# Optimization experiments

Measured on AMD Instinct MI355X. Metric: run time of the kernel, lower is better.

## Reference

```python
import jax, jax.numpy as jnp
import numpy as np

B, T = 64, 512
V, E = 512, 128      # dsl vocab, embedding dim
IMG = 1024           # img_repr_size
H = 512              # dsl_hidden_dim
A = 512              # n_actions
PAD = 0


def setup_inputs() -> dict:
    key = jax.random.key(0)
    ks = jax.random.split(key, 10)
    x1 = jax.random.normal(ks[0], (B, IMG), dtype=jnp.float32)
    x2 = jax.random.randint(ks[1], (B, T), 0, V)
    x2_lens = jax.random.randint(ks[2], (B,), 1, T + 1)
    s_in = 1.0 / np.sqrt(E + IMG)
    s_h = 1.0 / np.sqrt(H)
    emb = jax.random.normal(ks[3], (V, E), dtype=jnp.float32)
    emb = emb.at[PAD].set(0.0)  # padding_idx row is zero
    W_ih = jax.random.uniform(ks[4], (4 * H, E + IMG), jnp.float32, -s_h, s_h)
    W_hh = jax.random.uniform(ks[5], (4 * H, H), jnp.float32, -s_h, s_h)
    b_ih = jax.random.uniform(ks[6], (4 * H,), jnp.float32, -s_h, s_h)
    b_hh = jax.random.uniform(ks[7], (4 * H,), jnp.float32, -s_h, s_h)
    W_act = jax.random.uniform(ks[8], (A, H), jnp.float32, -s_h, s_h)
    b_act = jax.random.uniform(ks[9], (A,), jnp.float32, -s_h, s_h)
    return {"x1": x1, "x2": x2, "x2_lens": x2_lens, "emb": emb,
            "W_ih": W_ih, "W_hh": W_hh, "b_ih": b_ih, "b_hh": b_hh,
            "W_act": W_act, "b_act": b_act}


def reference(x1, x2, x2_lens, emb, W_ih, W_hh, b_ih, b_hh, W_act, b_act):
    # embed tokens and concat image repr at every timestep: [B, T, IMG+E]
    tok = emb[x2]                                        # [B, T, E]
    img = jnp.broadcast_to(x1[:, None, :], (B, T, IMG))  # [B, T, IMG]
    x = jnp.concatenate([img, tok], axis=2)              # [B, T, IMG+E]

    # precompute input-to-gate projections in one big GEMM
    gx = jnp.einsum('bti,gi->tbg', x, W_ih) + b_ih       # [T, B, 4H]

    def step(carry, gx_t):
        h, c = carry
        g = gx_t + h @ W_hh.T + b_hh                     # [B, 4H]
        i, f, gg, o = jnp.split(g, 4, axis=1)            # torch gate order i,f,g,o
        i = jax.nn.sigmoid(i); f = jax.nn.sigmoid(f)
        gg = jnp.tanh(gg); o = jax.nn.sigmoid(o)
        c = f * c + i * gg
        h = o * jnp.tanh(c)
        return (h, c), h

    h0 = jnp.zeros((B, H), jnp.float32)
    c0 = jnp.zeros((B, H), jnp.float32)
    (_, _), hs = jax.lax.scan(step, (h0, c0), gx)        # hs: [T, B, H]

    # hn = hidden state at each sequence's true last step (packed-seq semantics)
    idx = (x2_lens - 1).astype(jnp.int32)                # [B]
    hn = jnp.take_along_axis(hs.transpose(1, 0, 2), idx[:, None, None], axis=1)[:, 0, :]  # [B, H]

    nt = hn @ W_act.T + b_act                            # [B, A]
    return nt
```

## Files before the change

kernel.cpp:

```cpp
#include <hip/hip_runtime.h>
#include <cstdint>
#include <cstddef>


typedef _Float16     f16x8 __attribute__((ext_vector_type(8)));
typedef _Float16     f16x2 __attribute__((ext_vector_type(2)));
typedef float        f32x4 __attribute__((ext_vector_type(4)));
typedef float        f32x2 __attribute__((ext_vector_type(2)));
typedef unsigned int u32x4 __attribute__((ext_vector_type(4)));

#define TPB 256
#define NWG 64

#define WS_GX0   0
#define WS_P     524288
#define WS_HN    4718592
#define WS_HBUF  4849664
#define WS_FLAGS 4980736

__device__ __forceinline__ float sigm_(float x) { return 1.f / (1.f + __expf(-x)); }
__device__ __forceinline__ float tanh_(float x) {
    const float e = __expf(-2.f * fabsf(x));
    return copysignf((1.f - e) / (1.f + e), x);
}

__device__ __forceinline__ void st_ic_u32(unsigned int* p, unsigned int v) {
    __hip_atomic_store(p, v, __ATOMIC_RELAXED, __HIP_MEMORY_SCOPE_AGENT);
}
__device__ __forceinline__ unsigned int ld_ic_u32(const unsigned int* p) {
    return __hip_atomic_load(p, __ATOMIC_RELAXED, __HIP_MEMORY_SCOPE_AGENT);
}

__global__ void gemm_nt_bias(const float* __restrict__ A, int lda,
                             const float* __restrict__ B, int ldb,
                             float* __restrict__ C, int ldc, int K,
                             const float* __restrict__ bias1,
                             const float* __restrict__ bias2)
{
    __shared__ float As[32 * 68];
    __shared__ float Bs[32 * 68];
    const int tid = threadIdx.x;
    const int m0 = blockIdx.y * 64, n0 = blockIdx.x * 64;
    const int kchunk = K / gridDim.z;
    const int kbeg = blockIdx.z * kchunk, kend = kbeg + kchunk;
    const int tr = tid >> 4, tc = tid & 15;
    float acc[4][4] = {};

    for (int k0 = kbeg; k0 < kend; k0 += 32) {
        __syncthreads();
        #pragma unroll
        for (int idx = tid; idx < 2048; idx += TPB) {
            const int r = idx >> 5, kk = idx & 31;
            As[kk * 68 + r] = A[(size_t)(m0 + r) * lda + k0 + kk];
            Bs[kk * 68 + r] = B[(size_t)(n0 + r) * ldb + k0 + kk];
        }
        __syncthreads();
        #pragma unroll
        for (int kk = 0; kk < 32; ++kk) {
            const f32x4 a = *(const f32x4*)&As[kk * 68 + tr * 4];
            const f32x4 b = *(const f32x4*)&Bs[kk * 68 + tc * 4];
            #pragma unroll
            for (int i = 0; i < 4; ++i)
                #pragma unroll
                for (int j = 0; j < 4; ++j)
                    acc[i][j] = fmaf(a[i], b[j], acc[i][j]);
        }
    }

    const bool split = (gridDim.z > 1);
    #pragma unroll
    for (int i = 0; i < 4; ++i) {
        const int m = m0 + tr * 4 + i;
        #pragma unroll
        for (int j = 0; j < 4; ++j) {
            const int n = n0 + tc * 4 + j;
            float v = acc[i][j];
            if (blockIdx.z == 0) {
                if (bias1) v += bias1[n];
                if (bias2) v += bias2[n];
            }
            if (split) atomicAdd(&C[(size_t)m * ldc + n], v);
            else       C[(size_t)m * ldc + n] = v;
        }
    }
}

__global__ void __launch_bounds__(TPB, 1)
lstm_seq(const float* __restrict__ Whh,
         const float* __restrict__ GX0,
         const float* __restrict__ P,
         const int*   __restrict__ x2,
         const int*   __restrict__ lens,
         _Float16*    hbuf,
         float*       __restrict__ hn,
         unsigned int* flags)
{
    __shared__ float Spart[4 * 128 * 20];

    const int tid = threadIdx.x, wg = blockIdx.x;
    const int lane = tid & 63, wv = tid >> 6;
    const int BG = wg >> 4;
    const int CG = wg & 15;
    const int m16 = lane & 15, q = lane >> 4;

    const int bl  = tid >> 4;
    const int cq  = (tid & 15) * 2;
    const int b   = BG * 16 + bl;
    const int col = CG * 32 + cq;
    const int last = lens[b] - 1;
    const int* toks = x2 + b * 512;

    f32x2 gxv[4];
    {
        const float* gx = GX0 + (size_t)b * 2048 + col;
        #pragma unroll
        for (int g = 0; g < 4; ++g) gxv[g] = *(const f32x2*)(gx + g * 512);
    }

    { f16x2 z; z[0] = (_Float16)0.f; z[1] = (_Float16)0.f;
      st_ic_u32((unsigned int*)(hbuf + b * 512 + col),
                __builtin_bit_cast(unsigned int, z)); }
    __syncthreads();
    unsigned int* myflag = flags + (size_t)wg * 64;
    if (tid == 0) st_ic_u32(myflag, 1u);

    const unsigned int* pollp =
        flags + (size_t)(BG * 16 + wv * 4 + (lane & 3)) * 64;

    f16x8 bfr[8][4];
    #pragma unroll
    for (int n = 0; n < 8; ++n) {
        const int rr = n * 16 + m16;
        const int gr = (rr >> 5) * 512 + CG * 32 + (rr & 31);
        const float* wrow = Whh + (size_t)gr * 512 + wv * 128 + q * 8;
        #pragma unroll
        for (int ks = 0; ks < 4; ++ks) {
            const f32x4 w0 = *(const f32x4*)(wrow + ks * 32);
            const f32x4 w1 = *(const f32x4*)(wrow + ks * 32 + 4);
            f16x8 bv;
            #pragma unroll
            for (int e = 0; e < 4; ++e) {
                bv[e]     = (_Float16)w0[e];
                bv[4 + e] = (_Float16)w1[e];
            }
            bfr[n][ks] = bv;
        }
    }

    int tok1;
    f32x2 ppv[4];
    {
        const int tok0 = toks[0];
        const float* pp = P + (size_t)tok0 * 2048 + col;
        #pragma unroll
        for (int g = 0; g < 4; ++g) ppv[g] = *(const f32x2*)(pp + g * 512);
        tok1 = toks[1];
    }

    float c0 = 0.f, c1 = 0.f;

    for (int t = 0; t < 512; ++t) {
        const unsigned int tgt = (unsigned int)(t + 1);

        while (true) {
            const unsigned int v = ld_ic_u32(pollp);
            if (__all((int)(v >= tgt))) break;
        }
        asm volatile("" ::: "memory");

        const _Float16* hsrc = hbuf + (size_t)(t & 1) * (64 * 512);
        _Float16*       hdst = hbuf + (size_t)((t + 1) & 1) * (64 * 512);

        u32x4 a0, a1, a2, a3;
        {
            const _Float16* ap =
                hsrc + (BG * 16 + m16) * 512 + wv * 128 + q * 8;
            asm volatile(
                "global_load_dwordx4 %0, %4, off sc1\n\t"
                "global_load_dwordx4 %1, %4, off offset:64 sc1\n\t"
                "global_load_dwordx4 %2, %4, off offset:128 sc1\n\t"
                "global_load_dwordx4 %3, %4, off offset:192 sc1\n\t"
                "s_waitcnt vmcnt(0)"
                : "=&v"(a0), "=&v"(a1), "=&v"(a2), "=&v"(a3)
                : "v"(ap)
                : "memory");
        }
        f16x8 af[4] = {
            __builtin_bit_cast(f16x8, a0), __builtin_bit_cast(f16x8, a1),
            __builtin_bit_cast(f16x8, a2), __builtin_bit_cast(f16x8, a3)
        };

        f32x4 acc[8] = {};
        #pragma unroll
        for (int ks = 0; ks < 4; ++ks)
            #pragma unroll
            for (int n = 0; n < 8; ++n)
                acc[n] = __builtin_amdgcn_mfma_f32_16x16x32_f16(
                    af[ks], bfr[n][ks], acc[n], 0, 0, 0);

        {
            const int cl = lane & 15, r0 = (lane >> 4) * 4;
            #pragma unroll
            for (int n = 0; n < 8; ++n)
                *(f32x4*)&Spart[(wv * 128 + n * 16 + cl) * 20 + r0] = acc[n];
        }
        __syncthreads();

        f32x2 sv[4];
        #pragma unroll
        for (int g = 0; g < 4; ++g) {
            f32x2 s = {0.f, 0.f};
            #pragma unroll
            for (int w = 0; w < 4; ++w) {
                const int base = (w * 128 + g * 32 + cq) * 20 + bl;
                s[0] += Spart[base];
                s[1] += Spart[base + 20];
            }
            sv[g] = s;
        }

        float hv[2];
        #pragma unroll
        for (int p = 0; p < 2; ++p) {
            const float iv = sigm_(sv[0][p] + gxv[0][p] + ppv[0][p]);
            const float fv = sigm_(sv[1][p] + gxv[1][p] + ppv[1][p]);
            const float gv = tanh_(sv[2][p] + gxv[2][p] + ppv[2][p]);
            const float ov = sigm_(sv[3][p] + gxv[3][p] + ppv[3][p]);
            float& c = p ? c1 : c0;
            c = fv * c + iv * gv;
            hv[p] = ov * tanh_(c);
        }

        f16x2 hh; hh[0] = (_Float16)hv[0]; hh[1] = (_Float16)hv[1];
        st_ic_u32((unsigned int*)(hdst + b * 512 + col),
                  __builtin_bit_cast(unsigned int, hh));
        if (t == last) {
            f32x2 o; o[0] = hv[0]; o[1] = hv[1];
            *(f32x2*)(hn + (size_t)b * 512 + col) = o;
        }

        __syncthreads();
        if (tid == 0) st_ic_u32(myflag, (unsigned int)(t + 2));

        {
            const float* pn = P + (size_t)tok1 * 2048 + col;
            #pragma unroll
            for (int g = 0; g < 4; ++g)
                ppv[g] = *(const f32x2*)(pn + g * 512);
            tok1 = toks[t < 510 ? t + 2 : 511];
        }
    }
}

extern "C" void kernel_launch(void* const* d_in, const int* in_sizes, int n_in,
                              void* d_out, int out_size, void* d_ws, size_t ws_size,
                              hipStream_t stream)
{
    const float* x1    = (const float*)d_in[0];
    const int*   x2    = (const int*)  d_in[1];
    const int*   lens  = (const int*)  d_in[2];
    const float* emb   = (const float*)d_in[3];
    const float* W_ih  = (const float*)d_in[4];
    const float* W_hh  = (const float*)d_in[5];
    const float* b_ih  = (const float*)d_in[6];
    const float* b_hh  = (const float*)d_in[7];
    const float* W_act = (const float*)d_in[8];
    const float* b_act = (const float*)d_in[9];
    float* out = (float*)d_out;

    char* ws = (char*)d_ws;
    float*        GX0   = (float*)(ws + WS_GX0);
    float*        P     = (float*)(ws + WS_P);
    float*        hn    = (float*)(ws + WS_HN);
    _Float16*     hbuf  = (_Float16*)(ws + WS_HBUF);
    unsigned int* flags = (unsigned int*)(ws + WS_FLAGS);

    hipMemsetAsync(flags, 0, 16384, stream);
    hipMemsetAsync(GX0, 0, 64 * 2048 * sizeof(float), stream);
    hipMemsetAsync(out, 0, 64 * 512 * sizeof(float), stream);

    gemm_nt_bias<<<dim3(32, 1, 4), TPB, 0, stream>>>(
        x1, 1024, W_ih, 1152, GX0, 2048, 1024, b_ih, b_hh);
    gemm_nt_bias<<<dim3(32, 8, 1), TPB, 0, stream>>>(
        emb, 128, W_ih + 1024, 1152, P, 2048, 128, nullptr, nullptr);

    lstm_seq<<<NWG, TPB, 0, stream>>>(W_hh, GX0, P, x2, lens, hbuf, hn, flags);

    gemm_nt_bias<<<dim3(8, 1, 4), TPB, 0, stream>>>(
        hn, 512, W_act, 512, out, 512, 512, b_act, nullptr);
}
```

Baseline: 1.454 ms.

## Pack step tag with hidden values to replace flag polling and barrier

```diff
diff --git a/kernel.cpp b/kernel.cpp
--- a/kernel.cpp
+++ b/kernel.cpp
@@ -16,19 +16,11 @@
 #define WS_P     524288
 #define WS_HN    4718592
 #define WS_HBUF  4849664
-#define WS_FLAGS 4980736
 
 __device__ __forceinline__ float sigm_(float x) { return 1.f / (1.f + __expf(-x)); }
 __device__ __forceinline__ float tanh_(float x) {
     const float e = __expf(-2.f * fabsf(x));
     return copysignf((1.f - e) / (1.f + e), x);
-}
-
-__device__ __forceinline__ void st_ic_u32(unsigned int* p, unsigned int v) {
-    __hip_atomic_store(p, v, __ATOMIC_RELAXED, __HIP_MEMORY_SCOPE_AGENT);
-}
-__device__ __forceinline__ unsigned int ld_ic_u32(const unsigned int* p) {
-    return __hip_atomic_load(p, __ATOMIC_RELAXED, __HIP_MEMORY_SCOPE_AGENT);
 }
 
 __global__ void gemm_nt_bias(const float* __restrict__ A, int lda,
@@ -91,11 +83,10 @@
          const float* __restrict__ P,
          const int*   __restrict__ x2,
          const int*   __restrict__ lens,
-         _Float16*    hbuf,
-         float*       __restrict__ hn,
-         unsigned int* flags)
+         unsigned long long* hbuf,
+         float*       __restrict__ hn)
 {
-    __shared__ float Spart[4 * 128 * 20];
+    __shared__ float Spart[2 * 4 * 128 * 20];
 
     const int tid = threadIdx.x, wg = blockIdx.x;
     const int lane = tid & 63, wv = tid >> 6;
@@ -107,6 +98,7 @@
     const int cq  = (tid & 15) * 2;
     const int b   = BG * 16 + bl;
     const int col = CG * 32 + cq;
+    const int cp  = CG * 16 + (tid & 15);
     const int last = lens[b] - 1;
     const int* toks = x2 + b * 512;
 
@@ -117,15 +109,9 @@
         for (int g = 0; g < 4; ++g) gxv[g] = *(const f32x2*)(gx + g * 512);
     }
 
-    { f16x2 z; z[0] = (_Float16)0.f; z[1] = (_Float16)0.f;
-      st_ic_u32((unsigned int*)(hbuf + b * 512 + col),
-                __builtin_bit_cast(unsigned int, z)); }
-    __syncthreads();
-    unsigned int* myflag = flags + (size_t)wg * 64;
-    if (tid == 0) st_ic_u32(myflag, 1u);
-
-    const unsigned int* pollp =
-        flags + (size_t)(BG * 16 + wv * 4 + (lane & 3)) * 64;
+    __hip_atomic_store(hbuf + (size_t)b * 256 + cp,
+                       (unsigned long long)1u << 32,
+                       __ATOMIC_RELAXED, __HIP_MEMORY_SCOPE_AGENT);
 
     f16x8 bfr[8][4];
     #pragma unroll
@@ -147,6 +133,9 @@
         }
     }
 
+    const unsigned long long* abase =
+        hbuf + (size_t)(BG * 16 + m16) * 256 + wv * 64 + q * 4;
+
     int tok1;
     f32x2 ppv[4];
     {
@@ -161,33 +150,39 @@
 
     for (int t = 0; t < 512; ++t) {
         const unsigned int tgt = (unsigned int)(t + 1);
-
+        const unsigned long long* hs = abase + (size_t)(t & 1) * 16384;
+
+        u32x4 r0, r1, r2, r3, r4, r5, r6, r7;
         while (true) {
-            const unsigned int v = ld_ic_u32(pollp);
-            if (__all((int)(v >= tgt))) break;
-        }
-        asm volatile("" ::: "memory");
-
-        const _Float16* hsrc = hbuf + (size_t)(t & 1) * (64 * 512);
-        _Float16*       hdst = hbuf + (size_t)((t + 1) & 1) * (64 * 512);
-
-        u32x4 a0, a1, a2, a3;
-        {
-            const _Float16* ap =
-                hsrc + (BG * 16 + m16) * 512 + wv * 128 + q * 8;
             asm volatile(
-                "global_load_dwordx4 %0, %4, off sc1\n\t"
-                "global_load_dwordx4 %1, %4, off offset:64 sc1\n\t"
-                "global_load_dwordx4 %2, %4, off offset:128 sc1\n\t"
-                "global_load_dwordx4 %3, %4, off offset:192 sc1\n\t"
+                "global_load_dwordx4 %0, %8, off sc1\n\t"
+                "global_load_dwordx4 %1, %8, off offset:16 sc1\n\t"
+                "global_load_dwordx4 %2, %8, off offset:128 sc1\n\t"
+                "global_load_dwordx4 %3, %8, off offset:144 sc1\n\t"
+                "global_load_dwordx4 %4, %8, off offset:256 sc1\n\t"
+                "global_load_dwordx4 %5, %8, off offset:272 sc1\n\t"
+                "global_load_dwordx4 %6, %8, off offset:384 sc1\n\t"
+                "global_load_dwordx4 %7, %8, off offset:400 sc1\n\t"
                 "s_waitcnt vmcnt(0)"
-                : "=&v"(a0), "=&v"(a1), "=&v"(a2), "=&v"(a3)
-                : "v"(ap)
+                : "=&v"(r0), "=&v"(r1), "=&v"(r2), "=&v"(r3),
+                  "=&v"(r4), "=&v"(r5), "=&v"(r6), "=&v"(r7)
+                : "v"(hs)
                 : "memory");
-        }
+            const unsigned int d =
+                (r0[1] ^ tgt) | (r0[3] ^ tgt) | (r1[1] ^ tgt) | (r1[3] ^ tgt) |
+                (r2[1] ^ tgt) | (r2[3] ^ tgt) | (r3[1] ^ tgt) | (r3[3] ^ tgt) |
+                (r4[1] ^ tgt) | (r4[3] ^ tgt) | (r5[1] ^ tgt) | (r5[3] ^ tgt) |
+                (r6[1] ^ tgt) | (r6[3] ^ tgt) | (r7[1] ^ tgt) | (r7[3] ^ tgt);
+            if (__all((int)(d == 0u))) break;
+        }
+
+        u32x4 fw0 = {r0[0], r0[2], r1[0], r1[2]};
+        u32x4 fw1 = {r2[0], r2[2], r3[0], r3[2]};
+        u32x4 fw2 = {r4[0], r4[2], r5[0], r5[2]};
+        u32x4 fw3 = {r6[0], r6[2], r7[0], r7[2]};
         f16x8 af[4] = {
-            __builtin_bit_cast(f16x8, a0), __builtin_bit_cast(f16x8, a1),
-            __builtin_bit_cast(f16x8, a2), __builtin_bit_cast(f16x8, a3)
+            __builtin_bit_cast(f16x8, fw0), __builtin_bit_cast(f16x8, fw1),
+            __builtin_bit_cast(f16x8, fw2), __builtin_bit_cast(f16x8, fw3)
         };
 
         f32x4 acc[8] = {};
@@ -198,11 +193,12 @@
                 acc[n] = __builtin_amdgcn_mfma_f32_16x16x32_f16(
                     af[ks], bfr[n][ks], acc[n], 0, 0, 0);
 
+        float* sp = Spart + (t & 1) * 10240;
         {
-            const int cl = lane & 15, r0 = (lane >> 4) * 4;
+            const int cl = lane & 15, rr = (lane >> 4) * 4;
             #pragma unroll
             for (int n = 0; n < 8; ++n)
-                *(f32x4*)&Spart[(wv * 128 + n * 16 + cl) * 20 + r0] = acc[n];
+                *(f32x4*)&sp[(wv * 128 + n * 16 + cl) * 20 + rr] = acc[n];
         }
         __syncthreads();
 
@@ -213,8 +209,8 @@
             #pragma unroll
             for (int w = 0; w < 4; ++w) {
                 const int base = (w * 128 + g * 32 + cq) * 20 + bl;
-                s[0] += Spart[base];
-                s[1] += Spart[base + 20];
+                s[0] += sp[base];
+                s[1] += sp[base + 20];
             }
             sv[g] = s;
         }
@@ -232,15 +228,17 @@
         }
 
         f16x2 hh; hh[0] = (_Float16)hv[0]; hh[1] = (_Float16)hv[1];
-        st_ic_u32((unsigned int*)(hdst + b * 512 + col),
-                  __builtin_bit_cast(unsigned int, hh));
+        const unsigned long long pv =
+            ((unsigned long long)(unsigned int)(t + 2) << 32) |
+            (unsigned long long)__builtin_bit_cast(unsigned int, hh);
+        __hip_atomic_store(hbuf + (size_t)((t + 1) & 1) * 16384
+                                + (size_t)b * 256 + cp,
+                           pv, __ATOMIC_RELAXED, __HIP_MEMORY_SCOPE_AGENT);
+
         if (t == last) {
             f32x2 o; o[0] = hv[0]; o[1] = hv[1];
             *(f32x2*)(hn + (size_t)b * 512 + col) = o;
         }
-
-        __syncthreads();
-        if (tid == 0) st_ic_u32(myflag, (unsigned int)(t + 2));
 
         {
             const float* pn = P + (size_t)tok1 * 2048 + col;
@@ -269,13 +267,11 @@
     float* out = (float*)d_out;
 
     char* ws = (char*)d_ws;
-    float*        GX0   = (float*)(ws + WS_GX0);
-    float*        P     = (float*)(ws + WS_P);
-    float*        hn    = (float*)(ws + WS_HN);
-    _Float16*     hbuf  = (_Float16*)(ws + WS_HBUF);
-    unsigned int* flags = (unsigned int*)(ws + WS_FLAGS);
-
-    hipMemsetAsync(flags, 0, 16384, stream);
+    float*              GX0  = (float*)(ws + WS_GX0);
+    float*              P    = (float*)(ws + WS_P);
+    float*              hn   = (float*)(ws + WS_HN);
+    unsigned long long* hbuf = (unsigned long long*)(ws + WS_HBUF);
+
     hipMemsetAsync(GX0, 0, 64 * 2048 * sizeof(float), stream);
     hipMemsetAsync(out, 0, 64 * 512 * sizeof(float), stream);
 
@@ -284,7 +280,7 @@
     gemm_nt_bias<<<dim3(32, 8, 1), TPB, 0, stream>>>(
         emb, 128, W_ih + 1024, 1152, P, 2048, 128, nullptr, nullptr);
 
-    lstm_seq<<<NWG, TPB, 0, stream>>>(W_hh, GX0, P, x2, lens, hbuf, hn, flags);
+    lstm_seq<<<NWG, TPB, 0, stream>>>(W_hh, GX0, P, x2, lens, hbuf, hn);
 
     gemm_nt_bias<<<dim3(8, 1, 4), TPB, 0, stream>>>(
         hn, 512, W_act, 512, out, 512, 512, b_act, nullptr);
```

Measured after the change: 1.808 ms. 1.24x slower.
